# Optimization experiments

Hardware: AMD Instinct MI355X
Metric: run time of the kernel (lower is better)

Reference implementation:

```python
import jax, jax.numpy as jnp
import numpy as np

N_NODES = 50000
N_EDGES = 800000
D_IN = 64
D_HID = 128  # out_channels * expansion(2)
EPS_MSG = 1e-7
EPS_SOFTMAX = 1e-16
EPS_BN = 1e-5
N_LAYERS = 4


def mish(x):
    return x * jnp.tanh(jax.nn.softplus(x))


def setup_inputs() -> dict:
    key = jax.random.key(0)
    ks = jax.random.split(key, 8)
    x = jax.random.normal(ks[0], (N_NODES, D_IN), dtype=jnp.float32)
    edge_index = jax.random.randint(ks[1], (2, N_EDGES), 0, N_NODES, dtype=jnp.int64)
    # Per-layer GENConv MLP params: Linear(64->128), BN(128), ReLU, Linear(128->64)
    s1 = 1.0 / np.sqrt(D_IN)
    s2 = 1.0 / np.sqrt(D_HID)
    W1 = jax.random.uniform(ks[2], (N_LAYERS, D_IN, D_HID), jnp.float32, -s1, s1)
    b1 = jax.random.uniform(ks[3], (N_LAYERS, D_HID), jnp.float32, -s1, s1)
    gamma = jnp.ones((N_LAYERS, D_HID), jnp.float32)
    beta = jnp.zeros((N_LAYERS, D_HID), jnp.float32)
    W2 = jax.random.uniform(ks[4], (N_LAYERS, D_HID, D_IN), jnp.float32, -s2, s2)
    b2 = jax.random.uniform(ks[5], (N_LAYERS, D_IN), jnp.float32, -s2, s2)
    return {"x": x, "edge_index": edge_index, "W1": W1, "b1": b1,
            "gamma": gamma, "beta": beta, "W2": W2, "b2": b2}


def gen_conv(x, src, dst, W1, b1, gamma, beta, W2, b2):
    n = x.shape[0]
    # message: relu(x_j) + eps  -> [E, D]
    msg = jax.nn.relu(x[src]) + EPS_MSG
    # softmax aggregation (t=1) per destination node, per feature channel
    m = jax.ops.segment_max(msg, dst, num_segments=n)
    e = jnp.exp(msg - m[dst])
    denom = jax.ops.segment_sum(e, dst, num_segments=n)[dst] + EPS_SOFTMAX
    alpha = e / denom
    agg = jax.ops.segment_sum(msg * alpha, dst, num_segments=n)
    # residual with destination features, then 2-layer MLP w/ BatchNorm (train mode)
    h = agg + x
    h = h @ W1 + b1
    mu = jnp.mean(h, axis=0)
    var = jnp.var(h, axis=0)  # biased, as torch BN uses for normalization
    h = (h - mu) * jax.lax.rsqrt(var + EPS_BN) * gamma + beta
    h = jax.nn.relu(h)
    return h @ W2 + b2


def reference(x, edge_index, W1, b1, gamma, beta, W2, b2):
    src, dst = edge_index[0], edge_index[1]
    h = x
    for i in range(N_LAYERS):
        h = gen_conv(h, src, dst, W1[i], b1[i], gamma[i], beta[i], W2[i], b2[i])
        if i < N_LAYERS - 1:
            h = mish(h)
    return h
```

## Files before the change

kernel.cpp:

```cpp
#include <hip/hip_runtime.h>
#include <math.h>

#define N_NODES 50000
#define N_EDGES 800000
#define D_IN 64
#define D_HID 128
#define NPB 256
#define NB ((N_NODES + NPB - 1) / NPB)
#define P1_BLOCKS 800
#define EPB (N_EDGES / P1_BLOCKS)
#define CAP 8192
#define BCS 32
#define XCVT_B (N_NODES * D_IN / 4 / 256)

typedef unsigned short u16;
typedef unsigned int u32;
typedef __attribute__((ext_vector_type(8))) short short8;
typedef __attribute__((ext_vector_type(4))) float f32x4;

union U4S8 { uint4 u; short8 s; };

__device__ __forceinline__ float bf2f(u16 u) {
    u32 x = ((u32)u) << 16;
    float f; __builtin_memcpy(&f, &x, 4); return f;
}
__device__ __forceinline__ u16 f2bf(float f) {
    u32 x; __builtin_memcpy(&x, &f, 4);
    x += 0x7fffu + ((x >> 16) & 1u);
    return (u16)(x >> 16);
}
__device__ __forceinline__ u32 pk2(float a, float b) {
    return (u32)f2bf(a) | ((u32)f2bf(b) << 16);
}
__device__ __forceinline__ u32 relu2(u32 w) {
    u32 b = (w >> 15) & 0x00010001u;
    u32 m01 = b ^ 0x00010001u;
    u32 M = (m01 << 16) - m01;
    return w & M;
}

__global__ __launch_bounds__(256) void bin_pass1_kernel(const int* __restrict__ src,
                                                        const int* __restrict__ dst,
                                                        int* __restrict__ bcnt,
                                                        u32* __restrict__ ebuf,
                                                        float* __restrict__ bn,
                                                        int* __restrict__ esrc) {
    __shared__ int hist[NB];
    __shared__ int base[NB];
    const int tid = threadIdx.x;
    const int e0 = blockIdx.x * EPB, e1 = e0 + EPB;
    for (int b = tid; b < NB; b += 256) hist[b] = 0;
    if (blockIdx.x == 0) {
        ((float4*)bn)[tid] = make_float4(0.f, 0.f, 0.f, 0.f);
        if (tid < 16) esrc[N_EDGES + tid] = 0;
    }
    __syncthreads();
    for (int i = e0 + tid; i < e1; i += 256)
        atomicAdd(&hist[dst[i] >> 8], 1);
    __syncthreads();
    for (int b = tid; b < NB; b += 256) {
        base[b] = atomicAdd(&bcnt[b * BCS], hist[b]);
        hist[b] = 0;
    }
    __syncthreads();
    for (int i = e0 + tid; i < e1; i += 256) {
        int d = dst[i];
        int b = d >> 8;
        int slot = base[b] + atomicAdd(&hist[b], 1);
        ebuf[(size_t)b * CAP + slot] = ((u32)src[i] << 16) | (u32)d;
    }
}

__global__ __launch_bounds__(256) void p2xw_kernel(int* __restrict__ off,
                                                   const int* __restrict__ bcnt,
                                                   const u32* __restrict__ ebuf,
                                                   int* __restrict__ esrc,
                                                   const float* __restrict__ x,
                                                   u16* __restrict__ xb,
                                                   u16* __restrict__ rb,
                                                   const float* __restrict__ W1,
                                                   const float* __restrict__ W2,
                                                   u16* __restrict__ w1f,
                                                   u16* __restrict__ w2f) {
    const int tid = threadIdx.x;
    if (blockIdx.x < NB) {
        __shared__ int s[NPB];
        __shared__ int sdeg[NPB];
        __shared__ int soff[NPB];
        const int b = blockIdx.x;
        const int n0 = b * NPB;
        s[tid] = (tid < b) ? bcnt[tid * BCS] : 0;
        sdeg[tid] = 0;
        __syncthreads();
        #pragma unroll
        for (int o = 128; o > 0; o >>= 1) {
            if (tid < o) s[tid] += s[tid + o];
            __syncthreads();
        }
        const int sbase = s[0];
        const int cnt = bcnt[b * BCS];
        const u32* eb = ebuf + (size_t)b * CAP;
        for (int i = tid; i < cnt; i += 256)
            atomicAdd(&sdeg[(int)(eb[i] & 0xFFFFu) - n0], 1);
        __syncthreads();
        const int v = sdeg[tid];
        s[tid] = v;
        __syncthreads();
        #pragma unroll
        for (int o = 1; o < NPB; o <<= 1) {
            int u = (tid >= o) ? s[tid - o] : 0;
            __syncthreads();
            s[tid] += u;
            __syncthreads();
        }
        const int go = sbase + s[tid] - v;
        soff[tid] = go;
        if (n0 + tid < N_NODES) off[n0 + tid] = go;
        if (b == 0 && tid == 0) off[N_NODES] = N_EDGES;
        sdeg[tid] = 0;
        __syncthreads();
        for (int i = tid; i < cnt; i += 256) {
            u32 p = eb[i];
            int dl = (int)(p & 0xFFFFu) - n0;
            int slot = soff[dl] + atomicAdd(&sdeg[dl], 1);
            esrc[slot] = (int)(p >> 16);
        }
        return;
    }
    if (blockIdx.x < NB + XCVT_B) {
        int i = (blockIdx.x - NB) * 256 + tid;
        float4 v = ((const float4*)x)[i];
        u32 lo = pk2(v.x, v.y), hi = pk2(v.z, v.w);
        ((uint2*)xb)[i] = make_uint2(lo, hi);
        ((uint2*)rb)[i] = make_uint2(relu2(lo), relu2(hi));
        return;
    }
    const int b = blockIdx.x - NB - XCVT_B;
    const int L = b >> 1;
    if ((b & 1) == 0) {
        const float* W = W1 + (size_t)L * 64 * 128;
        u16* outp = w1f + (size_t)L * 8192;
        for (int idx = tid; idx < 1024; idx += 256) {
            int ln = idx & 63, th = idx >> 6;
            int half = th & 1, t = th >> 1;
            int k0 = half * 32 + (ln >> 4) * 8;
            int n = t * 16 + (ln & 15);
            uint4 o;
            o.x = pk2(W[(k0 + 0) * 128 + n], W[(k0 + 1) * 128 + n]);
            o.y = pk2(W[(k0 + 2) * 128 + n], W[(k0 + 3) * 128 + n]);
            o.z = pk2(W[(k0 + 4) * 128 + n], W[(k0 + 5) * 128 + n]);
            o.w = pk2(W[(k0 + 6) * 128 + n], W[(k0 + 7) * 128 + n]);
            *(uint4*)&outp[(size_t)idx * 8] = o;
        }
    } else {
        const float* W = W2 + (size_t)L * 128 * 64;
        u16* outp = w2f + (size_t)L * 8192;
        for (int idx = tid; idx < 1024; idx += 256) {
            int ln = idx & 63, th = idx >> 6;
            int ks = th & 3, t = th >> 2;
            int k0 = ks * 32 + (ln >> 4) * 8;
            int n = t * 16 + (ln & 15);
            uint4 o;
            o.x = pk2(W[(k0 + 0) * 64 + n], W[(k0 + 1) * 64 + n]);
            o.y = pk2(W[(k0 + 2) * 64 + n], W[(k0 + 3) * 64 + n]);
            o.z = pk2(W[(k0 + 4) * 64 + n], W[(k0 + 5) * 64 + n]);
            o.w = pk2(W[(k0 + 6) * 64 + n], W[(k0 + 7) * 64 + n]);
            *(uint4*)&outp[(size_t)idx * 8] = o;
        }
    }
}

__global__ __launch_bounds__(256) void agg_kernel(const u16* __restrict__ xb,
                                                  const u16* __restrict__ rb,
                                                  const int* __restrict__ off,
                                                  const int* __restrict__ esrc,
                                                  u16* __restrict__ h) {
    const int node = blockIdx.x * 4 + (threadIdx.x >> 6);
    const int ln = threadIdx.x & 63;
    const int jb = __builtin_amdgcn_readfirstlane(off[node]);
    const int je = __builtin_amdgcn_readfirstlane(off[node + 1]);
    const float xown = bf2f(xb[(size_t)node * 64 + ln]);
    float s0 = 0.f, s1 = 0.f, t0 = 0.f, t1 = 0.f;
    int j = jb;
    const int nfull = (je - jb) >> 4;
    for (int it = 0; it < nfull; ++it, j += 16) {
        #pragma unroll
        for (int kk = 0; kk < 16; kk += 2) {
            int i0 = esrc[j + kk];
            int i1 = esrc[j + kk + 1];
            float m0 = bf2f(rb[(size_t)i0 * 64 + ln]);
            float m1 = bf2f(rb[(size_t)i1 * 64 + ln]);
            float p0 = __expf(m0);
            float p1 = __expf(m1);
            s0 += p0; t0 = fmaf(m0, p0, t0);
            s1 += p1; t1 = fmaf(m1, p1, t1);
        }
    }
    const int rem = je - j;
    if (rem > 0) {
        #pragma unroll
        for (int kk = 0; kk < 16; kk += 2) {
            int i0 = esrc[j + kk];
            int i1 = esrc[j + kk + 1];
            float m0 = bf2f(rb[(size_t)i0 * 64 + ln]);
            float m1 = bf2f(rb[(size_t)i1 * 64 + ln]);
            float p0 = (kk < rem)     ? __expf(m0) : 0.f;
            float p1 = (kk + 1 < rem) ? __expf(m1) : 0.f;
            s0 += p0; t0 = fmaf(m0, p0, t0);
            s1 += p1; t1 = fmaf(m1, p1, t1);
        }
    }
    const float s = s0 + s1, t = t0 + t1;
    const float v = t / (s + 1e-16f) + 1e-7f + xown;
    h[(size_t)node * 64 + ln] = f2bf(v);
}

#define SC1 136
__global__ __launch_bounds__(256) void gemm1_kernel(const u16* __restrict__ A,
                                                    const u16* __restrict__ Wf,
                                                    const float* __restrict__ bias,
                                                    u16* __restrict__ Bout,
                                                    float* __restrict__ S,
                                                    float* __restrict__ Q) {
    __shared__ u16 sC[64 * SC1];
    __shared__ float sRed[2][4][128];
    const int tid = threadIdx.x;
    const int wave = tid >> 6, ln = tid & 63;
    const int lm = ln & 15, quad = ln >> 4;
    const int row0g = blockIdx.x * 64;
    const int row0 = row0g + wave * 16;
    const int rA = min(row0 + lm, N_NODES - 1);

    U4S8 a0, a1;
    a0.u = *(const uint4*)&A[(size_t)rA * 64 + quad * 8];
    a1.u = *(const uint4*)&A[(size_t)rA * 64 + 32 + quad * 8];

    f32x4 acc[8];
    #pragma unroll
    for (int t = 0; t < 8; t++) {
        float b = bias[t * 16 + lm];
        acc[t] = (f32x4){b, b, b, b};
    }
    #pragma unroll
    for (int t = 0; t < 8; t++) {
        U4S8 b0, b1;
        b0.u = *(const uint4*)&Wf[(size_t)((t * 2 + 0) * 64 + ln) * 8];
        b1.u = *(const uint4*)&Wf[(size_t)((t * 2 + 1) * 64 + ln) * 8];
        acc[t] = __builtin_amdgcn_mfma_f32_16x16x32_bf16(a0.s, b0.s, acc[t], 0, 0, 0);
        acc[t] = __builtin_amdgcn_mfma_f32_16x16x32_bf16(a1.s, b1.s, acc[t], 0, 0, 0);
    }
    const int rbase = row0 + quad * 4;
    #pragma unroll
    for (int t = 0; t < 8; t++) {
        float ss = 0.f, qq = 0.f;
        #pragma unroll
        for (int rg = 0; rg < 4; rg++) {
            if (rbase + rg < N_NODES) {
                float v = acc[t][rg];
                ss += v; qq = fmaf(v, v, qq);
            }
        }
        ss += __shfl_xor(ss, 16); ss += __shfl_xor(ss, 32);
        qq += __shfl_xor(qq, 16); qq += __shfl_xor(qq, 32);
        if (quad == 0) {
            sRed[0][wave][t * 16 + lm] = ss;
            sRed[1][wave][t * 16 + lm] = qq;
        }
    }
    const int lr0 = wave * 16 + quad * 4;
    #pragma unroll
    for (int t = 0; t < 8; t++) {
        #pragma unroll
        for (int rg = 0; rg < 4; rg++)
            sC[(lr0 + rg) * SC1 + t * 16 + lm] = f2bf(acc[t][rg]);
    }
    __syncthreads();
    const int c8 = (tid & 15) * 8;
    #pragma unroll
    for (int i = 0; i < 4; i++) {
        int lr = (tid >> 4) + i * 16;
        int r = row0g + lr;
        if (r < N_NODES)
            *(uint4*)&Bout[(size_t)r * 128 + c8] = *(const uint4*)&sC[lr * SC1 + c8];
    }
    if (tid < 128) {
        float v = sRed[0][0][tid] + sRed[0][1][tid] + sRed[0][2][tid] + sRed[0][3][tid];
        atomicAdd(&S[tid], v);
    } else {
        int c = tid - 128;
        float v = sRed[1][0][c] + sRed[1][1][c] + sRed[1][2][c] + sRed[1][3][c];
        atomicAdd(&Q[c], v);
    }
}

__device__ __forceinline__ float mish_f(float v) {
    if (v > 30.f) return v;
    float u = __expf(v);
    float t = (u + 1.f) * (u + 1.f);
    return v * (t - 1.f) / (t + 1.f);
}

#define SC2B 72
#define SC2F 68
__global__ __launch_bounds__(256) void gemm2_kernel(const u16* __restrict__ H,
                                                    const float* __restrict__ S,
                                                    const float* __restrict__ Q,
                                                    const float* __restrict__ gamma,
                                                    const float* __restrict__ beta,
                                                    const u16* __restrict__ Wf,
                                                    const float* __restrict__ bias,
                                                    float* __restrict__ outf,
                                                    u16* __restrict__ xb,
                                                    u16* __restrict__ rb,
                                                    int dobf16) {
    __shared__ float sss[256];
    __shared__ __align__(16) char sCraw[64 * SC2F * 4];
    u16* sCb = (u16*)sCraw;
    float* sCf = (float*)sCraw;
    const int tid = threadIdx.x;
    if (tid < 128) {
        float mean = S[tid] * (1.f / N_NODES);
        float var = fmaxf(Q[tid] * (1.f / N_NODES) - mean * mean, 0.f);
        float sc = gamma[tid] * rsqrtf(var + 1e-5f);
        sss[tid] = sc;
        sss[128 + tid] = beta[tid] - mean * sc;
    }
    __syncthreads();
    const int wave = tid >> 6, ln = tid & 63;
    const int lm = ln & 15, quad = ln >> 4;
    const int row0g = blockIdx.x * 64;
    const int row0 = row0g + wave * 16;
    const int rA = min(row0 + lm, N_NODES - 1);

    f32x4 acc[4];
    #pragma unroll
    for (int t = 0; t < 4; t++) {
        float b = bias[t * 16 + lm];
        acc[t] = (f32x4){b, b, b, b};
    }
    #pragma unroll
    for (int ks = 0; ks < 4; ks++) {
        const int k0 = ks * 32 + quad * 8;
        U4S8 h8;
        h8.u = *(const uint4*)&H[(size_t)rA * 128 + k0];
        U4S8 a;
        #pragma unroll
        for (int j2 = 0; j2 < 4; j2++) {
            int k = k0 + 2 * j2;
            float v0 = fmaxf(fmaf(bf2f((u16)h8.s[2 * j2]),     sss[k],     sss[128 + k]),     0.f);
            float v1 = fmaxf(fmaf(bf2f((u16)h8.s[2 * j2 + 1]), sss[k + 1], sss[128 + k + 1]), 0.f);
            ((u32*)&a.u)[j2] = pk2(v0, v1);
        }
        #pragma unroll
        for (int t = 0; t < 4; t++) {
            U4S8 b;
            b.u = *(const uint4*)&Wf[(size_t)((t * 4 + ks) * 64 + ln) * 8];
            acc[t] = __builtin_amdgcn_mfma_f32_16x16x32_bf16(a.s, b.s, acc[t], 0, 0, 0);
        }
    }
    const int lr0 = wave * 16 + quad * 4;
    if (dobf16) {
        #pragma unroll
        for (int t = 0; t < 4; t++) {
            #pragma unroll
            for (int rg = 0; rg < 4; rg++)
                sCb[(lr0 + rg) * SC2B + t * 16 + lm] = f2bf(mish_f(acc[t][rg]));
        }
        __syncthreads();
        const int c8 = (tid & 7) * 8;
        #pragma unroll
        for (int i = 0; i < 2; i++) {
            int lr = (tid >> 3) + i * 32;
            int r = row0g + lr;
            if (r < N_NODES) {
                uint4 val = *(const uint4*)&sCb[lr * SC2B + c8];
                *(uint4*)&xb[(size_t)r * 64 + c8] = val;
                uint4 rv;
                rv.x = relu2(val.x); rv.y = relu2(val.y);
                rv.z = relu2(val.z); rv.w = relu2(val.w);
                *(uint4*)&rb[(size_t)r * 64 + c8] = rv;
            }
        }
    } else {
        #pragma unroll
        for (int t = 0; t < 4; t++) {
            #pragma unroll
            for (int rg = 0; rg < 4; rg++)
                sCf[(lr0 + rg) * SC2F + t * 16 + lm] = acc[t][rg];
        }
        __syncthreads();
        const int c8 = (tid & 7) * 8;
        #pragma unroll
        for (int i = 0; i < 2; i++) {
            int lr = (tid >> 3) + i * 32;
            int r = row0g + lr;
            if (r < N_NODES) {
                *(float4*)&outf[(size_t)r * 64 + c8]     = *(const float4*)&sCf[lr * SC2F + c8];
                *(float4*)&outf[(size_t)r * 64 + c8 + 4] = *(const float4*)&sCf[lr * SC2F + c8 + 4];
            }
        }
    }
}


extern "C" void kernel_launch(void* const* d_in, const int* in_sizes, int n_in,
                              void* d_out, int out_size, void* d_ws, size_t ws_size,
                              hipStream_t stream) {
    const float* x     = (const float*)d_in[0];
    const int*   ei    = (const int*)d_in[1];
    const float* W1    = (const float*)d_in[2];
    const float* b1    = (const float*)d_in[3];
    const float* gamma = (const float*)d_in[4];
    const float* beta  = (const float*)d_in[5];
    const float* W2    = (const float*)d_in[6];
    const float* b2    = (const float*)d_in[7];
    float* out = (float*)d_out;

    const int* src = ei;
    const int* dst = ei + N_EDGES;

    char* base = (char*)d_ws;
    size_t o = 0;
    auto take = [&](size_t bytes) -> char* {
        char* p = base + o;
        o = (o + bytes + 255) & ~(size_t)255;
        return p;
    };
    int* bcnt    = (int*)take((size_t)NB * BCS * 4);
    int* off     = (int*)take((size_t)(N_NODES + 1) * 4);
    int* esrc    = (int*)take((size_t)(N_EDGES + 16) * 4);
    u32* ebuf    = (u32*)take((size_t)NB * CAP * 4);
    float* bn    = (float*)take(1024 * 4);
    u16* w1f     = (u16*)take((size_t)4 * 8192 * 2);
    u16* w2f     = (u16*)take((size_t)4 * 8192 * 2);
    u16* xbuf    = (u16*)take((size_t)N_NODES * D_IN * 2);
    u16* rbuf    = (u16*)take((size_t)N_NODES * D_IN * 2);
    u16* hbuf    = (u16*)take((size_t)N_NODES * D_IN * 2);
    u16* h1buf   = (u16*)take((size_t)N_NODES * D_HID * 2);

    hipMemsetAsync(bcnt, 0, (size_t)NB * BCS * 4, stream);
    bin_pass1_kernel<<<P1_BLOCKS, 256, 0, stream>>>(src, dst, bcnt, ebuf, bn, esrc);
    p2xw_kernel<<<NB + XCVT_B + 8, 256, 0, stream>>>(off, bcnt, ebuf, esrc,
                                                     x, xbuf, rbuf,
                                                     W1, W2, w1f, w2f);

    const int NBLK = (N_NODES + 63) / 64;
    const int ABLK = (N_NODES + 3) / 4;
    for (int L = 0; L < 4; L++) {
        float* Sb = bn + L * 256;
        float* Qb = Sb + 128;
        agg_kernel<<<ABLK, 256, 0, stream>>>(xbuf, rbuf, off, esrc, hbuf);
        gemm1_kernel<<<NBLK, 256, 0, stream>>>(
            hbuf, w1f + (size_t)L * 8192, b1 + (size_t)L * D_HID, h1buf,
            Sb, Qb);
        gemm2_kernel<<<NBLK, 256, 0, stream>>>(
            h1buf, Sb, Qb, gamma + (size_t)L * D_HID, beta + (size_t)L * D_HID,
            w2f + (size_t)L * 8192, b2 + (size_t)L * D_IN,
            out, xbuf, rbuf, (L < 3) ? 1 : 0);
    }
}
```

Measured before the change: 351.1 us.

## Fuse the two MLP GEMMs via a grid-wide semaphore barrier for BatchNorm stats

Merges gemm1 and gemm2 into one persistent-style kernel. Each block keeps its hidden 64x128 tile in shared memory, adds its BN partial sums, then spins on a global atomic counter until all blocks have contributed before normalizing and running the second GEMM. This removes the round trip of the hidden activation buffer through global memory and one kernel launch per layer. In exchange it depends on all 782 blocks being co-resident (launch_bounds 256,4), and every block stalls at the barrier.

New measurement: 412.1 us. +17.4%, slower.

```diff
diff --git a/kernel.cpp b/kernel.cpp
--- a/kernel.cpp
+++ b/kernel.cpp
@@ -12,6 +12,7 @@
 #define CAP 8192
 #define BCS 32
 #define XCVT_B (N_NODES * D_IN / 4 / 256)
+#define NBLK ((N_NODES + 63) / 64)
 
 typedef unsigned short u16;
 typedef unsigned int u32;
@@ -44,6 +45,7 @@
                                                         int* __restrict__ bcnt,
                                                         u32* __restrict__ ebuf,
                                                         float* __restrict__ bn,
+                                                        int* __restrict__ sem,
                                                         int* __restrict__ esrc) {
     __shared__ int hist[NB];
     __shared__ int base[NB];
@@ -53,6 +55,7 @@
     if (blockIdx.x == 0) {
         ((float4*)bn)[tid] = make_float4(0.f, 0.f, 0.f, 0.f);
         if (tid < 16) esrc[N_EDGES + tid] = 0;
+        if (tid < 8) sem[tid] = 0;
     }
     __syncthreads();
     for (int i = e0 + tid; i < e1; i += 256)
@@ -216,14 +219,35 @@
 }
 
 #define SC1 136
-__global__ __launch_bounds__(256) void gemm1_kernel(const u16* __restrict__ A,
-                                                    const u16* __restrict__ Wf,
-                                                    const float* __restrict__ bias,
-                                                    u16* __restrict__ Bout,
-                                                    float* __restrict__ S,
-                                                    float* __restrict__ Q) {
-    __shared__ u16 sC[64 * SC1];
+#define SC2B 72
+#define SC2F 68
+__device__ __forceinline__ float mish_f(float v) {
+    if (v > 30.f) return v;
+    float u = __expf(v);
+    float t = (u + 1.f) * (u + 1.f);
+    return v * (t - 1.f) / (t + 1.f);
+}
+
+__global__ __launch_bounds__(256, 4) void gemm12_kernel(const u16* __restrict__ A,
+                                                        const u16* __restrict__ W1f,
+                                                        const float* __restrict__ b1v,
+                                                        float* __restrict__ S,
+                                                        float* __restrict__ Q,
+                                                        const float* __restrict__ gamma,
+                                                        const float* __restrict__ beta,
+                                                        const u16* __restrict__ W2f,
+                                                        const float* __restrict__ b2v,
+                                                        float* __restrict__ outf,
+                                                        u16* __restrict__ xb,
+                                                        u16* __restrict__ rb,
+                                                        int* __restrict__ sem,
+                                                        int dobf16) {
+    __shared__ __align__(16) char sCraw[64 * SC1 * 2];
+    u16* sC = (u16*)sCraw;
+    u16* sCb = (u16*)sCraw;
+    float* sCf = (float*)sCraw;
     __shared__ float sRed[2][4][128];
+    __shared__ float sss[256];
     const int tid = threadIdx.x;
     const int wave = tid >> 6, ln = tid & 63;
     const int lm = ln & 15, quad = ln >> 4;
@@ -238,16 +262,16 @@
     f32x4 acc[8];
     #pragma unroll
     for (int t = 0; t < 8; t++) {
-        float b = bias[t * 16 + lm];
+        float b = b1v[t * 16 + lm];
         acc[t] = (f32x4){b, b, b, b};
     }
     #pragma unroll
     for (int t = 0; t < 8; t++) {
-        U4S8 b0, b1;
-        b0.u = *(const uint4*)&Wf[(size_t)((t * 2 + 0) * 64 + ln) * 8];
-        b1.u = *(const uint4*)&Wf[(size_t)((t * 2 + 1) * 64 + ln) * 8];
+        U4S8 b0, b1w;
+        b0.u  = *(const uint4*)&W1f[(size_t)((t * 2 + 0) * 64 + ln) * 8];
+        b1w.u = *(const uint4*)&W1f[(size_t)((t * 2 + 1) * 64 + ln) * 8];
         acc[t] = __builtin_amdgcn_mfma_f32_16x16x32_bf16(a0.s, b0.s, acc[t], 0, 0, 0);
-        acc[t] = __builtin_amdgcn_mfma_f32_16x16x32_bf16(a1.s, b1.s, acc[t], 0, 0, 0);
+        acc[t] = __builtin_amdgcn_mfma_f32_16x16x32_bf16(a1.s, b1w.s, acc[t], 0, 0, 0);
     }
     const int rbase = row0 + quad * 4;
     #pragma unroll
@@ -275,14 +299,6 @@
             sC[(lr0 + rg) * SC1 + t * 16 + lm] = f2bf(acc[t][rg]);
     }
     __syncthreads();
-    const int c8 = (tid & 15) * 8;
-    #pragma unroll
-    for (int i = 0; i < 4; i++) {
-        int lr = (tid >> 4) + i * 16;
-        int r = row0g + lr;
-        if (r < N_NODES)
-            *(uint4*)&Bout[(size_t)r * 128 + c8] = *(const uint4*)&sC[lr * SC1 + c8];
-    }
     if (tid < 128) {
         float v = sRed[0][0][tid] + sRed[0][1][tid] + sRed[0][2][tid] + sRed[0][3][tid];
         atomicAdd(&S[tid], v);
@@ -291,80 +307,59 @@
         float v = sRed[1][0][c] + sRed[1][1][c] + sRed[1][2][c] + sRed[1][3][c];
         atomicAdd(&Q[c], v);
     }
-}
-
-__device__ __forceinline__ float mish_f(float v) {
-    if (v > 30.f) return v;
-    float u = __expf(v);
-    float t = (u + 1.f) * (u + 1.f);
-    return v * (t - 1.f) / (t + 1.f);
-}
-
-#define SC2B 72
-#define SC2F 68
-__global__ __launch_bounds__(256) void gemm2_kernel(const u16* __restrict__ H,
-                                                    const float* __restrict__ S,
-                                                    const float* __restrict__ Q,
-                                                    const float* __restrict__ gamma,
-                                                    const float* __restrict__ beta,
-                                                    const u16* __restrict__ Wf,
-                                                    const float* __restrict__ bias,
-                                                    float* __restrict__ outf,
-                                                    u16* __restrict__ xb,
-                                                    u16* __restrict__ rb,
-                                                    int dobf16) {
-    __shared__ float sss[256];
-    __shared__ __align__(16) char sCraw[64 * SC2F * 4];
-    u16* sCb = (u16*)sCraw;
-    float* sCf = (float*)sCraw;
-    const int tid = threadIdx.x;
+    __syncthreads();
+    if (tid == 0) {
+        __hip_atomic_fetch_add(sem, 1, __ATOMIC_ACQ_REL, __HIP_MEMORY_SCOPE_AGENT);
+        while (__hip_atomic_load(sem, __ATOMIC_ACQUIRE, __HIP_MEMORY_SCOPE_AGENT) < NBLK)
+            __builtin_amdgcn_s_sleep(8);
+    }
+    __syncthreads();
+
     if (tid < 128) {
-        float mean = S[tid] * (1.f / N_NODES);
-        float var = fmaxf(Q[tid] * (1.f / N_NODES) - mean * mean, 0.f);
+        float Sv = __hip_atomic_load(&S[tid], __ATOMIC_RELAXED, __HIP_MEMORY_SCOPE_AGENT);
+        float Qv = __hip_atomic_load(&Q[tid], __ATOMIC_RELAXED, __HIP_MEMORY_SCOPE_AGENT);
+        float mean = Sv * (1.f / N_NODES);
+        float var = fmaxf(Qv * (1.f / N_NODES) - mean * mean, 0.f);
         float sc = gamma[tid] * rsqrtf(var + 1e-5f);
         sss[tid] = sc;
         sss[128 + tid] = beta[tid] - mean * sc;
     }
-    __syncthreads();
-    const int wave = tid >> 6, ln = tid & 63;
-    const int lm = ln & 15, quad = ln >> 4;
-    const int row0g = blockIdx.x * 64;
-    const int row0 = row0g + wave * 16;
-    const int rA = min(row0 + lm, N_NODES - 1);
-
-    f32x4 acc[4];
+    U4S8 h8[4];
+    #pragma unroll
+    for (int ks = 0; ks < 4; ks++)
+        h8[ks].u = *(const uint4*)&sC[(size_t)(wave * 16 + lm) * SC1 + ks * 32 + quad * 8];
+    __syncthreads();
+
+    f32x4 acc2[4];
     #pragma unroll
     for (int t = 0; t < 4; t++) {
-        float b = bias[t * 16 + lm];
-        acc[t] = (f32x4){b, b, b, b};
+        float b = b2v[t * 16 + lm];
+        acc2[t] = (f32x4){b, b, b, b};
     }
     #pragma unroll
     for (int ks = 0; ks < 4; ks++) {
         const int k0 = ks * 32 + quad * 8;
-        U4S8 h8;
-        h8.u = *(const uint4*)&H[(size_t)rA * 128 + k0];
         U4S8 a;
         #pragma unroll
         for (int j2 = 0; j2 < 4; j2++) {
             int k = k0 + 2 * j2;
-            float v0 = fmaxf(fmaf(bf2f((u16)h8.s[2 * j2]),     sss[k],     sss[128 + k]),     0.f);
-            float v1 = fmaxf(fmaf(bf2f((u16)h8.s[2 * j2 + 1]), sss[k + 1], sss[128 + k + 1]), 0.f);
+            float v0 = fmaxf(fmaf(bf2f((u16)h8[ks].s[2 * j2]),     sss[k],     sss[128 + k]),     0.f);
+            float v1 = fmaxf(fmaf(bf2f((u16)h8[ks].s[2 * j2 + 1]), sss[k + 1], sss[128 + k + 1]), 0.f);
             ((u32*)&a.u)[j2] = pk2(v0, v1);
         }
         #pragma unroll
         for (int t = 0; t < 4; t++) {
             U4S8 b;
-            b.u = *(const uint4*)&Wf[(size_t)((t * 4 + ks) * 64 + ln) * 8];
-            acc[t] = __builtin_amdgcn_mfma_f32_16x16x32_bf16(a.s, b.s, acc[t], 0, 0, 0);
-        }
-    }
-    const int lr0 = wave * 16 + quad * 4;
+            b.u = *(const uint4*)&W2f[(size_t)((t * 4 + ks) * 64 + ln) * 8];
+            acc2[t] = __builtin_amdgcn_mfma_f32_16x16x32_bf16(a.s, b.s, acc2[t], 0, 0, 0);
+        }
+    }
     if (dobf16) {
         #pragma unroll
         for (int t = 0; t < 4; t++) {
             #pragma unroll
             for (int rg = 0; rg < 4; rg++)
-                sCb[(lr0 + rg) * SC2B + t * 16 + lm] = f2bf(mish_f(acc[t][rg]));
+                sCb[(lr0 + rg) * SC2B + t * 16 + lm] = f2bf(mish_f(acc2[t][rg]));
         }
         __syncthreads();
         const int c8 = (tid & 7) * 8;
@@ -386,7 +381,7 @@
         for (int t = 0; t < 4; t++) {
             #pragma unroll
             for (int rg = 0; rg < 4; rg++)
-                sCf[(lr0 + rg) * SC2F + t * 16 + lm] = acc[t][rg];
+                sCf[(lr0 + rg) * SC2F + t * 16 + lm] = acc2[t][rg];
         }
         __syncthreads();
         const int c8 = (tid & 7) * 8;
@@ -431,31 +426,28 @@
     int* esrc    = (int*)take((size_t)(N_EDGES + 16) * 4);
     u32* ebuf    = (u32*)take((size_t)NB * CAP * 4);
     float* bn    = (float*)take(1024 * 4);
+    int* sem     = (int*)take(8 * 4);
     u16* w1f     = (u16*)take((size_t)4 * 8192 * 2);
     u16* w2f     = (u16*)take((size_t)4 * 8192 * 2);
     u16* xbuf    = (u16*)take((size_t)N_NODES * D_IN * 2);
     u16* rbuf    = (u16*)take((size_t)N_NODES * D_IN * 2);
     u16* hbuf    = (u16*)take((size_t)N_NODES * D_IN * 2);
-    u16* h1buf   = (u16*)take((size_t)N_NODES * D_HID * 2);
 
     hipMemsetAsync(bcnt, 0, (size_t)NB * BCS * 4, stream);
-    bin_pass1_kernel<<<P1_BLOCKS, 256, 0, stream>>>(src, dst, bcnt, ebuf, bn, esrc);
+    bin_pass1_kernel<<<P1_BLOCKS, 256, 0, stream>>>(src, dst, bcnt, ebuf, bn, sem, esrc);
     p2xw_kernel<<<NB + XCVT_B + 8, 256, 0, stream>>>(off, bcnt, ebuf, esrc,
                                                      x, xbuf, rbuf,
                                                      W1, W2, w1f, w2f);
 
-    const int NBLK = (N_NODES + 63) / 64;
     const int ABLK = (N_NODES + 3) / 4;
     for (int L = 0; L < 4; L++) {
         float* Sb = bn + L * 256;
         float* Qb = Sb + 128;
         agg_kernel<<<ABLK, 256, 0, stream>>>(xbuf, rbuf, off, esrc, hbuf);
-        gemm1_kernel<<<NBLK, 256, 0, stream>>>(
-            hbuf, w1f + (size_t)L * 8192, b1 + (size_t)L * D_HID, h1buf,
-            Sb, Qb);
-        gemm2_kernel<<<NBLK, 256, 0, stream>>>(
-            h1buf, Sb, Qb, gamma + (size_t)L * D_HID, beta + (size_t)L * D_HID,
+        gemm12_kernel<<<NBLK, 256, 0, stream>>>(
+            hbuf, w1f + (size_t)L * 8192, b1 + (size_t)L * D_HID,
+            Sb, Qb, gamma + (size_t)L * D_HID, beta + (size_t)L * D_HID,
             w2f + (size_t)L * 8192, b2 + (size_t)L * D_IN,
-            out, xbuf, rbuf, (L < 3) ? 1 : 0);
-    }
-}
+            out, xbuf, rbuf, sem + L, (L < 3) ? 1 : 0);
+    }
+}
```
